# Kernel tuning notes

Measured on AMD Instinct MI355X. Metric: run time of the kernel, lower is better.

## Reference

```python
import jax, jax.numpy as jnp
import numpy as np

HEAD = 8
C = 32  # dhead
SCALE = 0.17677669529663687  # 1/sqrt(32)


def setup_inputs() -> dict:
    key = jax.random.key(0)
    k1, k2, k3, k4 = jax.random.split(key, 4)
    N, S, R, M = 1, 256, 384, 256
    msa_repr = jax.random.normal(k1, (N, S, R, M), dtype=jnp.float32)
    # 0.02 init scale keeps softmax logits / sigmoid pre-activations in a sane range
    gate_proj = jax.random.normal(k2, (M, M), dtype=jnp.float32) * 0.02
    qkv_proj = jax.random.normal(k3, (M, 3 * M), dtype=jnp.float32) * 0.02
    out_proj = jax.random.normal(k4, (M, M), dtype=jnp.float32) * 0.02
    return {"msa_repr": msa_repr, "gate_proj": gate_proj, "qkv_proj": qkv_proj, "out_proj": out_proj}


def reference(msa_repr, gate_proj, qkv_proj, out_proj):
    # col_attn: permute [N,S,R,M] -> [N,R,S,M]; attention runs over the residue axis S
    x = jnp.transpose(msa_repr, (0, 2, 1, 3))  # [N,R,S,M]
    N, R, S, M = x.shape
    gate = jax.nn.sigmoid(x @ gate_proj).reshape(N, R, S, HEAD, C)
    q, k, v = jnp.split(x @ qkv_proj, 3, axis=-1)  # each [N,R,S,M]
    q = q.reshape(N, R, S, HEAD, C)
    k = k.reshape(N, R, S, HEAD, C)
    v = v.reshape(N, R, S, HEAD, C)
    sim = jnp.einsum('nrihc,nrjhc->nrhij', q, k) * jnp.float32(SCALE)  # [N,R,H,S,S]
    attn = jax.nn.softmax(sim, axis=-1)
    out = jnp.einsum('nrhij,nrjhc->nrihc', attn, v) * gate  # [N,R,S,H,C]
    out = out.reshape(N, R, S, HEAD * C) @ out_proj  # [N,R,S,M]
    return jnp.transpose(out, (0, 2, 1, 3))  # back to [N,S,R,M]
```

## Files before the change

### kernel.cpp

```cpp
#include <hip/hip_runtime.h>
#include <hip/hip_bf16.h>

#define R_DIM 384
#define S_DIM 256
#define M_DIM 256

typedef __attribute__((ext_vector_type(4))) float  f32x4;
typedef __attribute__((ext_vector_type(4))) float  fvec4;
typedef __attribute__((ext_vector_type(8))) short  short8;
typedef __attribute__((ext_vector_type(4))) short  short4v;
typedef __attribute__((ext_vector_type(2))) int    i32x2;

__device__ __forceinline__ short f2bf(float f) {
    __hip_bfloat16 h = __float2bfloat16(f);
    return __builtin_bit_cast(short, h);
}
__device__ __forceinline__ float bf2f(short s) {
    return __bfloat162float(__builtin_bit_cast(__hip_bfloat16, s));
}

#if __has_builtin(__builtin_amdgcn_mfma_f32_16x16x16bf16_1k)
__device__ __forceinline__ f32x4 mfma16(short4v a, short4v b, f32x4 c) {
    return __builtin_amdgcn_mfma_f32_16x16x16bf16_1k(a, b, c, 0, 0, 0);
}
#else
__device__ __forceinline__ f32x4 mfma16(short4v a, short4v b, f32x4 c) {
    f32x4 d;
    asm volatile("v_mfma_f32_16x16x16_bf16 %0, %1, %2, %3\n\t"
                 "s_nop 7\n\ts_nop 7"
                 : "=&v"(d) : "v"(a), "v"(b), "v"(c));
    return d;
}
#endif

__device__ __forceinline__ void gload_lds16(const void* gsrc, void* ldst) {
    __builtin_amdgcn_global_load_lds(
        (const __attribute__((address_space(1))) unsigned int*)gsrc,
        (__attribute__((address_space(3))) unsigned int*)ldst, 16, 0, 0);
}

#define QSCALE (0.17677669529663687f * 1.4426950408889634f)

__global__ __launch_bounds__(256) void k_prep(
    const float* __restrict__ gp, const float* __restrict__ qkvp,
    const float* __restrict__ op, short* __restrict__ Wt1,
    short* __restrict__ Wot)
{
    __shared__ float tile[64][65];
    const int tx = threadIdx.x & 63, ty = threadIdx.x >> 6;
    const int k0 = blockIdx.x * 64;
    const int j0 = blockIdx.y * 64;
    const float* src; int ld, cb;
    if (j0 < 256)       { src = gp;   ld = 256; cb = j0; }
    else if (j0 < 1024) { src = qkvp; ld = 768; cb = j0 - 256; }
    else                { src = op;   ld = 256; cb = j0 - 1024; }
    for (int q = 0; q < 16; ++q) {
        const int kk = q * 4 + ty;
        tile[kk][tx] = src[(k0 + kk) * ld + cb + tx];
    }
    __syncthreads();
    for (int q = 0; q < 16; ++q) {
        const int jj = q * 4 + ty;
        const int jglob = j0 + jj;
        const float scl = (jglob >= 256 && jglob < 512) ? QSCALE : 1.0f;
        const float val = tile[tx][jj] * scl;
        if (jglob < 1024) Wt1[jglob * 256 + k0 + tx] = f2bf(val);
        else              Wot[(jglob - 1024) * 256 + k0 + tx] = f2bf(val);
    }
}

__global__ __launch_bounds__(256, 3) void k_qkvgate(
    const float* __restrict__ msa, const short* __restrict__ Wt1,
    short* __restrict__ gate, short* __restrict__ qb,
    short* __restrict__ kb, short* __restrict__ vb)
{
    __shared__ __align__(16) char Al[64 * 512];
    __shared__ __align__(16) short Bl[2][128 * 32];
    const int tid = threadIdx.x;
    const int l = tid & 63, w = tid >> 6;
    const int wr = w >> 1, wc = w & 1;
    const int rowBase = blockIdx.x * 64;

    {
        const int arow0 = tid >> 6;
        const int col4  = (tid & 63) * 4;
        const int slot  = (tid & 63) >> 1;
        const int sub   = (tid & 63) & 1;
        for (int ii = 0; ii < 16; ++ii) {
            const int a_r = ii * 4 + arow0;
            const int i = rowBase + a_r;
            const int rr = i >> 8, ss = i & 255;
            fvec4 vv = *(const fvec4*)(msa + ((ss * R_DIM + rr) << 8) + col4);
            short4v b4;
            b4.x = f2bf(vv.x); b4.y = f2bf(vv.y);
            b4.z = f2bf(vv.z); b4.w = f2bf(vv.w);
            *(short4v*)(Al + a_r * 512 + ((slot ^ (a_r & 7)) << 4) + sub * 8) = b4;
        }
    }

    auto stageB = [&](int tt, short* buf) {
        const int cb = (tt >> 3) * 128, k0 = (tt & 7) * 32;
        #pragma unroll
        for (int r = 0; r < 2; ++r) {
            const int L = r * 256 + w * 64 + l;
            const int row = L >> 2, psl = L & 3;
            const int gsl = psl ^ ((row >> 1) & 3);
            gload_lds16(Wt1 + (cb + row) * 256 + k0 + gsl * 8,
                        buf + (r * 256 + w * 64) * 8);
        }
    };

    stageB(0, (short*)Bl[0]);
    __syncthreads();

    short8 af[8][2];
    #pragma unroll
    for (int kc = 0; kc < 8; ++kc) {
        const int aslot = kc * 4 + (l >> 4);
        #pragma unroll
        for (int it = 0; it < 2; ++it) {
            const int row = wr * 32 + it * 16 + (l & 15);
            af[kc][it] = *(const short8*)(Al + row * 512 + ((aslot ^ (row & 7)) << 4));
        }
    }

    short* AlT = (short*)Al;
    const int rr_blk = rowBase >> 8;
    const int ssBase = rowBase & 255;

    f32x4 acc[2][4] = {};
    for (int ct = 0; ct < 8; ++ct) {
        #pragma unroll
        for (int kc = 0; kc < 8; ++kc) {
            const int t = ct * 8 + kc;
            if (t + 1 < 64) stageB(t + 1, (short*)Bl[(kc + 1) & 1]);

            const short* Bb = (const short*)Bl[kc & 1];
            short8 bfr[4];
            #pragma unroll
            for (int jt = 0; jt < 4; ++jt) {
                const int row = wc * 64 + jt * 16 + (l & 15);
                const int psl = (l >> 4) ^ ((row >> 1) & 3);
                bfr[jt] = *(const short8*)(Bb + row * 32 + psl * 8);
            }
            #pragma unroll
            for (int it = 0; it < 2; ++it)
                #pragma unroll
                for (int jt = 0; jt < 4; ++jt)
                    acc[it][jt] = __builtin_amdgcn_mfma_f32_16x16x32_bf16(
                        af[kc][it], bfr[jt], acc[it][jt], 0, 0, 0);

            __syncthreads();
        }
        const int colBase = ct * 128;
        const int sel = ct >> 1;
        if (sel < 3) {
            short* dst = (sel == 0) ? gate : (sel == 1) ? qb : kb;
            #pragma unroll
            for (int it = 0; it < 2; ++it) {
                const int base_i = rowBase + wr * 32 + it * 16 + ((l >> 4) << 2);
                #pragma unroll
                for (int reg = 0; reg < 4; ++reg) {
                    const int i = base_i + reg;
                    const int rr = i >> 8, ss = i & 255;
                    #pragma unroll
                    for (int jt = 0; jt < 4; ++jt) {
                        const int jg = colBase + wc * 64 + jt * 16 + (l & 15);
                        const int jj = jg & 255;
                        const int h = jj >> 5, c = jj & 31;
                        float vv = acc[it][jt][reg];
                        if (sel == 0) vv = 1.0f / (1.0f + __builtin_amdgcn_exp2f(-vv * 1.4426950408889634f));
                        dst[(((rr << 3) + h) * 256 + ss) * 32 + c] = f2bf(vv);
                    }
                }
            }
        } else {
            const int jjBase = (colBase & 255);
            #pragma unroll
            for (int it = 0; it < 2; ++it) {
                const int ssL0 = wr * 32 + it * 16 + ((l >> 4) << 2);
                #pragma unroll
                for (int reg = 0; reg < 4; ++reg) {
                    #pragma unroll
                    for (int jt = 0; jt < 4; ++jt) {
                        const int jjL = wc * 64 + jt * 16 + (l & 15);
                        AlT[jjL * 72 + ssL0 + reg] = f2bf(acc[it][jt][reg]);
                    }
                }
            }
            __syncthreads();
            #pragma unroll
            for (int q = 0; q < 4; ++q) {
                const int cid = q * 256 + tid;
                const int jjL = cid >> 3, sc = cid & 7;
                short8 vv8 = *(const short8*)(&AlT[jjL * 72 + sc * 8]);
                const int jj = jjBase + jjL;
                const int h = jj >> 5, c = jj & 31;
                const int pp = (rr_blk << 3) + h;
                *(short8*)(vb + (pp << 13) + (c << 8) + ssBase + sc * 8) = vv8;
            }
        }
        #pragma unroll
        for (int it = 0; it < 2; ++it)
            #pragma unroll
            for (int jt = 0; jt < 4; ++jt)
                acc[it][jt] = (f32x4){0.f, 0.f, 0.f, 0.f};
    }
}

__global__ __launch_bounds__(256) void k_attn(
    short* qo, const short* __restrict__ kb, const short* __restrict__ vb,
    const short* __restrict__ gate)
{
    const int tid = threadIdx.x;
    const int l = tid & 63, w = tid >> 6;
    const int p = blockIdx.x;
    short* qg = qo + p * 8192;
    const short* kg = kb + p * 8192;
    const short* vg = vb + p * 8192;
    const short* gg = gate + p * 8192;
    const int r = l & 15, g = l >> 4;
    const int c0 = g * 8;

    short8 qf[4];
    #pragma unroll
    for (int it = 0; it < 4; ++it) {
        const int s = w * 64 + it * 16 + r;
        qf[it] = *(const short8*)(qg + s * 32 + c0);
    }

    f32x4 oacc[4][2] = {};
    f32x4 ssum[4] = {};
    short4v ones4;
    ones4.x = (short)0x3F80; ones4.y = (short)0x3F80;
    ones4.z = (short)0x3F80; ones4.w = (short)0x3F80;

    for (int ch = 0; ch < 4; ++ch) {
        const int j0 = ch * 64;
        short8 kf[4];
        #pragma unroll
        for (int jt = 0; jt < 4; ++jt) {
            const int row = j0 + jt * 16 + r;
            kf[jt] = *(const short8*)(kg + row * 32 + c0);
        }
        #pragma unroll
        for (int jt = 0; jt < 4; ++jt) {
            f32x4 st[4];
            #pragma unroll
            for (int it = 0; it < 4; ++it)
                st[it] = __builtin_amdgcn_mfma_f32_16x16x32_bf16(
                    kf[jt], qf[it], (f32x4){0.f, 0.f, 0.f, 0.f}, 0, 0, 0);
            short4v pf[4];
            #pragma unroll
            for (int it = 0; it < 4; ++it) {
                const unsigned u0 =
                    (unsigned)(unsigned short)f2bf(__builtin_amdgcn_exp2f(st[it][0])) |
                    ((unsigned)(unsigned short)f2bf(__builtin_amdgcn_exp2f(st[it][1])) << 16);
                const unsigned u1 =
                    (unsigned)(unsigned short)f2bf(__builtin_amdgcn_exp2f(st[it][2])) |
                    ((unsigned)(unsigned short)f2bf(__builtin_amdgcn_exp2f(st[it][3])) << 16);
                i32x2 t; t.x = (int)u0; t.y = (int)u1;
                pf[it] = __builtin_bit_cast(short4v, t);
            }
            short4v vf[2];
            #pragma unroll
            for (int cti = 0; cti < 2; ++cti)
                vf[cti] = *(const short4v*)(
                    vg + (cti * 16 + r) * 256 + j0 + jt * 16 + g * 4);
            #pragma unroll
            for (int it = 0; it < 4; ++it) {
                #pragma unroll
                for (int cti = 0; cti < 2; ++cti)
                    oacc[it][cti] = mfma16(pf[it], vf[cti], oacc[it][cti]);
                ssum[it] = mfma16(pf[it], ones4, ssum[it]);
            }
        }
    }
    #pragma unroll
    for (int it = 0; it < 4; ++it) {
        #pragma unroll
        for (int reg = 0; reg < 4; ++reg) {
            const float inv = 1.0f / ssum[it][reg];
            const int s = w * 64 + it * 16 + (g << 2) + reg;
            #pragma unroll
            for (int cti = 0; cti < 2; ++cti) {
                const int c = cti * 16 + r;
                const float gv = bf2f(gg[s * 32 + c]);
                qg[s * 32 + c] = f2bf(oacc[it][cti][reg] * inv * gv);
            }
        }
    }
}

__global__ __launch_bounds__(256, 4) void k_out(
    const short* __restrict__ ao, const short* __restrict__ Wot,
    float* __restrict__ out)
{
    __shared__ __align__(16) short Bl[2][128 * 32];
    const int tid = threadIdx.x;
    const int l = tid & 63, w = tid >> 6;
    const int wr = w >> 1, wc = w & 1;
    const int rowBase = blockIdx.y * 128;
    const int colBase = blockIdx.x * 128;

    auto stageB = [&](int kc, short* buf) {
        const int k0 = kc * 32;
        #pragma unroll
        for (int r = 0; r < 2; ++r) {
            const int L = r * 256 + w * 64 + l;
            const int row = L >> 2, psl = L & 3;
            const int gsl = psl ^ ((row >> 1) & 3);
            gload_lds16(Wot + (colBase + row) * 256 + k0 + gsl * 8,
                        buf + (r * 256 + w * 64) * 8);
        }
    };

    stageB(0, (short*)Bl[0]);
    __syncthreads();

    f32x4 acc[4][4] = {};
    #pragma unroll
    for (int kc = 0; kc < 8; ++kc) {
        if (kc + 1 < 8) stageB(kc + 1, (short*)Bl[(kc + 1) & 1]);

        short8 af[4];
        #pragma unroll
        for (int it = 0; it < 4; ++it) {
            const int i = rowBase + wr * 64 + it * 16 + (l & 15);
            const int rr = i >> 8, ss = i & 255;
            af[it] = *(const short8*)(ao + (((rr << 3) + kc) * 256 + ss) * 32 + (l >> 4) * 8);
        }
        const short* Bb = (const short*)Bl[kc & 1];
        short8 bfr[4];
        #pragma unroll
        for (int jt = 0; jt < 4; ++jt) {
            const int row = wc * 64 + jt * 16 + (l & 15);
            const int psl = (l >> 4) ^ ((row >> 1) & 3);
            bfr[jt] = *(const short8*)(Bb + row * 32 + psl * 8);
        }
        #pragma unroll
        for (int it = 0; it < 4; ++it)
            #pragma unroll
            for (int jt = 0; jt < 4; ++jt)
                acc[it][jt] = __builtin_amdgcn_mfma_f32_16x16x32_bf16(
                    af[it], bfr[jt], acc[it][jt], 0, 0, 0);

        __syncthreads();
    }
    #pragma unroll
    for (int it = 0; it < 4; ++it) {
        const int base_i = rowBase + wr * 64 + it * 16 + ((l >> 4) << 2);
        #pragma unroll
        for (int reg = 0; reg < 4; ++reg) {
            const int i = base_i + reg;
            const int rr = i >> 8, ss = i & 255;
            #pragma unroll
            for (int jt = 0; jt < 4; ++jt) {
                const int m = colBase + wc * 64 + jt * 16 + (l & 15);
                out[((ss * R_DIM + rr) << 8) + m] = acc[it][jt][reg];
            }
        }
    }
}

extern "C" void kernel_launch(void* const* d_in, const int* in_sizes, int n_in,
                              void* d_out, int out_size, void* d_ws, size_t ws_size,
                              hipStream_t stream) {
    const float* msa  = (const float*)d_in[0];
    const float* gp   = (const float*)d_in[1];
    const float* qkvp = (const float*)d_in[2];
    const float* op   = (const float*)d_in[3];
    float* out = (float*)d_out;
    char* ws = (char*)d_ws;

    const size_t SZ = 50331648;
    short* Wt1  = (short*)ws;
    short* Wot  = (short*)(ws + 524288);
    short* gate = (short*)(ws + 655360);
    short* qb   = (short*)(ws + 655360 + 1 * SZ);
    short* kb   = (short*)(ws + 655360 + 2 * SZ);
    short* vb   = (short*)(ws + 655360 + 3 * SZ);

    k_prep<<<dim3(4, 20), 256, 0, stream>>>(gp, qkvp, op, Wt1, Wot);
    k_qkvgate<<<dim3(1536), 256, 0, stream>>>(msa, Wt1, gate, qb, kb, vb);
    k_attn<<<dim3(3072), 256, 0, stream>>>(qb, kb, vb, gate);
    k_out<<<dim3(2, 768), 256, 0, stream>>>(qb, Wot, out);
}
```

Baseline: 220.3 us.

## Deepen B staging to four buffers and halve A LDS staging in qkvgate

The QKV/gate projection kernel now stages the A tile (converted msa rows) in two 32-row halves through a smaller shared buffer, with each wave-row loading its fragments from the half it owns. The B weight tiles move from double to quadruple buffering, prefetching two k-steps ahead and syncing once per two k-chunks. The aim is fewer barriers, more latency hiding for the global-to-LDS weight loads, and lower shared-memory use for A. The cost is extra barriers during the A load phase, and the total LDS footprint changes, which may affect occupancy.

```diff
diff --git a/kernel.cpp b/kernel.cpp
--- a/kernel.cpp
+++ b/kernel.cpp
@@ -74,29 +74,12 @@
     short* __restrict__ gate, short* __restrict__ qb,
     short* __restrict__ kb, short* __restrict__ vb)
 {
-    __shared__ __align__(16) char Al[64 * 512];
-    __shared__ __align__(16) short Bl[2][128 * 32];
+    __shared__ __align__(16) short Ah[128 * 72];
+    __shared__ __align__(16) short Bl[4][128 * 32];
     const int tid = threadIdx.x;
     const int l = tid & 63, w = tid >> 6;
     const int wr = w >> 1, wc = w & 1;
     const int rowBase = blockIdx.x * 64;
-
-    {
-        const int arow0 = tid >> 6;
-        const int col4  = (tid & 63) * 4;
-        const int slot  = (tid & 63) >> 1;
-        const int sub   = (tid & 63) & 1;
-        for (int ii = 0; ii < 16; ++ii) {
-            const int a_r = ii * 4 + arow0;
-            const int i = rowBase + a_r;
-            const int rr = i >> 8, ss = i & 255;
-            fvec4 vv = *(const fvec4*)(msa + ((ss * R_DIM + rr) << 8) + col4);
-            short4v b4;
-            b4.x = f2bf(vv.x); b4.y = f2bf(vv.y);
-            b4.z = f2bf(vv.z); b4.w = f2bf(vv.w);
-            *(short4v*)(Al + a_r * 512 + ((slot ^ (a_r & 7)) << 4) + sub * 8) = b4;
-        }
-    }
 
     auto stageB = [&](int tt, short* buf) {
         const int cb = (tt >> 3) * 128, k0 = (tt & 7) * 32;
@@ -111,45 +94,72 @@
     };
 
     stageB(0, (short*)Bl[0]);
-    __syncthreads();
+    stageB(1, (short*)Bl[1]);
 
     short8 af[8][2];
-    #pragma unroll
-    for (int kc = 0; kc < 8; ++kc) {
-        const int aslot = kc * 4 + (l >> 4);
-        #pragma unroll
-        for (int it = 0; it < 2; ++it) {
-            const int row = wr * 32 + it * 16 + (l & 15);
-            af[kc][it] = *(const short8*)(Al + row * 512 + ((aslot ^ (row & 7)) << 4));
-        }
-    }
-
-    short* AlT = (short*)Al;
+    for (int h = 0; h < 2; ++h) {
+        {
+            const int arow0 = tid >> 6;
+            const int col4  = (tid & 63) * 4;
+            const int slot  = (tid & 63) >> 1;
+            const int sub   = (tid & 63) & 1;
+            for (int ii = 0; ii < 8; ++ii) {
+                const int a_r = ii * 4 + arow0;
+                const int i = rowBase + h * 32 + a_r;
+                const int rr = i >> 8, ss = i & 255;
+                fvec4 vv = *(const fvec4*)(msa + ((ss * R_DIM + rr) << 8) + col4);
+                short4v b4;
+                b4.x = f2bf(vv.x); b4.y = f2bf(vv.y);
+                b4.z = f2bf(vv.z); b4.w = f2bf(vv.w);
+                *(short4v*)((char*)Ah + a_r * 512 + ((slot ^ (a_r & 7)) << 4) + sub * 8) = b4;
+            }
+        }
+        __syncthreads();
+        if (wr == h) {
+            #pragma unroll
+            for (int kc = 0; kc < 8; ++kc) {
+                const int aslot = kc * 4 + (l >> 4);
+                #pragma unroll
+                for (int it = 0; it < 2; ++it) {
+                    const int row = it * 16 + (l & 15);
+                    af[kc][it] = *(const short8*)((char*)Ah + row * 512 +
+                                                  ((aslot ^ (row & 7)) << 4));
+                }
+            }
+        }
+        __syncthreads();
+    }
+
+    short* AlT = (short*)Ah;
     const int rr_blk = rowBase >> 8;
     const int ssBase = rowBase & 255;
 
     f32x4 acc[2][4] = {};
     for (int ct = 0; ct < 8; ++ct) {
         #pragma unroll
-        for (int kc = 0; kc < 8; ++kc) {
-            const int t = ct * 8 + kc;
-            if (t + 1 < 64) stageB(t + 1, (short*)Bl[(kc + 1) & 1]);
-
-            const short* Bb = (const short*)Bl[kc & 1];
-            short8 bfr[4];
-            #pragma unroll
-            for (int jt = 0; jt < 4; ++jt) {
-                const int row = wc * 64 + jt * 16 + (l & 15);
-                const int psl = (l >> 4) ^ ((row >> 1) & 3);
-                bfr[jt] = *(const short8*)(Bb + row * 32 + psl * 8);
-            }
-            #pragma unroll
-            for (int it = 0; it < 2; ++it)
-                #pragma unroll
-                for (int jt = 0; jt < 4; ++jt)
-                    acc[it][jt] = __builtin_amdgcn_mfma_f32_16x16x32_bf16(
-                        af[kc][it], bfr[jt], acc[it][jt], 0, 0, 0);
-
+        for (int ip = 0; ip < 4; ++ip) {
+            const int t0 = ct * 8 + ip * 2;
+            if (t0 + 2 < 64) stageB(t0 + 2, (short*)Bl[(t0 + 2) & 3]);
+            if (t0 + 3 < 64) stageB(t0 + 3, (short*)Bl[(t0 + 3) & 3]);
+
+            #pragma unroll
+            for (int u = 0; u < 2; ++u) {
+                const int kc = ip * 2 + u;
+                const short* Bb = (const short*)Bl[(t0 + u) & 3];
+                short8 bfr[4];
+                #pragma unroll
+                for (int jt = 0; jt < 4; ++jt) {
+                    const int row = wc * 64 + jt * 16 + (l & 15);
+                    const int psl = (l >> 4) ^ ((row >> 1) & 3);
+                    bfr[jt] = *(const short8*)(Bb + row * 32 + psl * 8);
+                }
+                #pragma unroll
+                for (int it = 0; it < 2; ++it)
+                    #pragma unroll
+                    for (int jt = 0; jt < 4; ++jt)
+                        acc[it][jt] = __builtin_amdgcn_mfma_f32_16x16x32_bf16(
+                            af[kc][it], bfr[jt], acc[it][jt], 0, 0, 0);
+            }
             __syncthreads();
         }
         const int colBase = ct * 128;
```

New measurement: 209.5 us (median of 2 runs). -4.9%, faster.
